# Kernel optimization log

Hardware: AMD Instinct MI355X
Metric: run time of the kernel (lower is better)

Reference implementation:

```python
import jax, jax.numpy as jnp
import numpy as np


def setup_inputs() -> dict:
    key = jax.random.key(0)
    k1, k2 = jax.random.split(key)
    N, H, K, E = 8192, 4096, 2, 64
    x = jax.random.normal(k1, (N, H), dtype=jnp.float32)
    row_idx = jnp.arange(N * K, dtype=jnp.int32).reshape(N, K)
    expert_idx = jax.random.randint(k2, (N, K), 0, E, dtype=jnp.int32)
    return {"x": x, "row_idx": row_idx, "expert_idx": expert_idx, "active_num": N * K}


def reference(x, row_idx, expert_idx, active_num):
    # x: [N, H]; row_idx, expert_idx: [N, K]
    N, H = x.shape
    K = expert_idx.shape[1]
    NK = N * K

    expert_flat = expert_idx.reshape(-1)  # [N*K]
    row_flat = row_idx.reshape(-1)        # [N*K]

    # Step 1: stable sort by expert id, carry row indices
    sorted_indices = jnp.argsort(expert_flat, stable=True)
    expanded_expert_idx = expert_flat[sorted_indices]
    dst_to_src = row_flat[sorted_indices]

    # Step 2: invert the permutation: src_to_dst[dst_to_src[i]] = i
    expanded_row_idx = jnp.zeros(NK, dtype=jnp.int32).at[dst_to_src].set(
        jnp.arange(NK, dtype=jnp.int32)
    )

    # Step 3: gather x rows; dst_to_src % N gives the original token row
    expanded_x = x[dst_to_src % N]  # [N*K, H]

    return expanded_x, expanded_row_idx, expanded_expert_idx
```

## Files before the change

kernel.cpp:

```cpp
#include <hip/hip_runtime.h>
#include <hip/hip_bf16.h>

#define TPB 256
#define NEXPERT 64

typedef float f32x4 __attribute__((ext_vector_type(4)));


__global__ void k_hist(const int* __restrict__ expert, int NK, int NB,
                       int* __restrict__ counts) {
    __shared__ int h[NEXPERT];
    const int b = blockIdx.x;
    for (int e = threadIdx.x; e < NEXPERT; e += blockDim.x) h[e] = 0;
    __syncthreads();
    const int i = b * TPB + threadIdx.x;
    if (i < NK) atomicAdd(&h[expert[i]], 1);
    __syncthreads();
    for (int e = threadIdx.x; e < NEXPERT; e += blockDim.x)
        counts[e * NB + b] = h[e];
}

__global__ void k_scan(int* __restrict__ counts, int M) {
    __shared__ int s[1024];
    const int t = threadIdx.x;
    const int nt = blockDim.x;
    const int ipt = (M + nt - 1) / nt;
    int v[8];
    int sum = 0;
    for (int j = 0; j < ipt; ++j) {
        const int idx = t * ipt + j;
        v[j] = (idx < M) ? counts[idx] : 0;
        sum += v[j];
    }
    s[t] = sum;
    __syncthreads();
    for (int off = 1; off < nt; off <<= 1) {
        const int x = (t >= off) ? s[t - off] : 0;
        __syncthreads();
        s[t] += x;
        __syncthreads();
    }
    int base = (t == 0) ? 0 : s[t - 1];
    for (int j = 0; j < ipt; ++j) {
        const int idx = t * ipt + j;
        const int c = v[j];
        if (idx < M) counts[idx] = base;
        base += c;
    }
}

__global__ void k_scatter(const int* __restrict__ expert,
                          const int* __restrict__ rowi,
                          int NK, int NB,
                          const int* __restrict__ base,
                          float* __restrict__ out_row,
                          float* __restrict__ out_expert,
                          int* __restrict__ dst_of_r) {
    __shared__ int h[TPB / 64][NEXPERT + 1];
    const int b = blockIdx.x;
    const int tid = threadIdx.x;
    const int w = tid >> 6;
    const int lane = tid & 63;
    const int i = b * TPB + tid;
    const bool valid = (i < NK);
    const int e = valid ? expert[i] : NEXPERT;

    for (int idx = tid; idx < (TPB / 64) * (NEXPERT + 1); idx += TPB)
        (&h[0][0])[idx] = 0;
    __syncthreads();

    unsigned long long mask = ~0ull;
#pragma unroll
    for (int bit = 0; bit < 7; ++bit) {
        const unsigned long long bv = __ballot((e >> bit) & 1);
        mask &= ((e >> bit) & 1) ? bv : ~bv;
    }
    const int rank_w = __popcll(mask & ((1ull << lane) - 1ull));
    const int cnt_w  = __popcll(mask);
    if (rank_w == 0) h[w][e] = cnt_w;
    __syncthreads();

    if (valid) {
        int rank = rank_w;
        for (int w2 = 0; w2 < w; ++w2) rank += h[w2][e];
        const int dst = base[e * NB + b] + rank;
        const int r = rowi[i];
        out_expert[dst] = (float)e;
        out_row[r] = (float)dst;
        dst_of_r[r] = dst;
    }
}

template <int K>
__global__ void k_gatherT(const float* __restrict__ x,
                          const int* __restrict__ dst_of_r,
                          float* __restrict__ out_x, int H, int N) {
    const int t = blockIdx.x;
    const f32x4* __restrict__ src = (const f32x4*)(x + (size_t)t * (size_t)H);
    size_t ob[K];
#pragma unroll
    for (int kk = 0; kk < K; ++kk)
        ob[kk] = (size_t)dst_of_r[t + kk * N] * (size_t)H;
    const int n4 = H >> 2;
    for (int j = threadIdx.x; j < n4; j += blockDim.x) {
        const f32x4 v = src[j];
#pragma unroll
        for (int kk = 0; kk < K; ++kk)
            __builtin_nontemporal_store(v, (f32x4*)(out_x + ob[kk]) + j);
    }
}

__global__ void k_gather_gen(const float* __restrict__ x,
                             const int* __restrict__ dst_of_r,
                             float* __restrict__ out_x, int H, int N, int K) {
    const int t = blockIdx.x;
    const f32x4* __restrict__ src = (const f32x4*)(x + (size_t)t * (size_t)H);
    const int n4 = H >> 2;
    for (int kk = 0; kk < K; ++kk) {
        const size_t ob = (size_t)dst_of_r[t + kk * N] * (size_t)H;
        for (int j = threadIdx.x; j < n4; j += blockDim.x)
            __builtin_nontemporal_store(src[j], (f32x4*)(out_x + ob) + j);
    }
}

extern "C" void kernel_launch(void* const* d_in, const int* in_sizes, int n_in,
                              void* d_out, int out_size, void* d_ws, size_t ws_size,
                              hipStream_t stream) {
    const float* x    = (const float*)d_in[0];
    const int*   rowi = (const int*)d_in[1];
    const int*   expi = (const int*)d_in[2];

    const int NK = in_sizes[1];
    const int H  = (out_size - 2 * NK) / NK;
    const int N  = in_sizes[0] / H;
    const int K  = NK / N;
    const int NB = (NK + TPB - 1) / TPB;

    float* out_x      = (float*)d_out;
    float* out_row    = out_x + (size_t)NK * (size_t)H;
    float* out_expert = out_row + NK;

    int* counts   = (int*)d_ws;
    int* dst_of_r = counts + NEXPERT * NB;

    k_hist   <<<NB, TPB, 0, stream>>>(expi, NK, NB, counts);
    k_scan   <<<1, 1024, 0, stream>>>(counts, NEXPERT * NB);
    k_scatter<<<NB, TPB, 0, stream>>>(expi, rowi, NK, NB, counts,
                                      out_row, out_expert, dst_of_r);

    switch (K) {
        case 1: k_gatherT<1><<<N, TPB, 0, stream>>>(x, dst_of_r, out_x, H, N); break;
        case 2: k_gatherT<2><<<N, TPB, 0, stream>>>(x, dst_of_r, out_x, H, N); break;
        case 3: k_gatherT<3><<<N, TPB, 0, stream>>>(x, dst_of_r, out_x, H, N); break;
        case 4: k_gatherT<4><<<N, TPB, 0, stream>>>(x, dst_of_r, out_x, H, N); break;
        default: k_gather_gen<<<N, TPB, 0, stream>>>(x, dst_of_r, out_x, H, N, K); break;
    }
}
```

Before: 77.62 us.

## Fuse prefix scan into scatter kernel, recomputing scan redundantly per block

Removes the single-block scan kernel and has every scatter block load the full histogram (64*NB counts) into shared memory and compute the exclusive prefix scan itself. This drops one kernel launch and the serial dependency on a one-block kernel. In exchange, every block redoes the whole scan and needs about 33 KB of dynamic LDS, which lowers occupancy. The scan also assumes M is divisible by TPB.

Result: faster. 75.39 us, median of 2 (-2.9%).

```diff
diff --git a/kernel.cpp b/kernel.cpp
--- a/kernel.cpp
+++ b/kernel.cpp
@@ -20,54 +20,49 @@
         counts[e * NB + b] = h[e];
 }
 
-__global__ void k_scan(int* __restrict__ counts, int M) {
-    __shared__ int s[1024];
-    const int t = threadIdx.x;
-    const int nt = blockDim.x;
-    const int ipt = (M + nt - 1) / nt;
-    int v[8];
-    int sum = 0;
-    for (int j = 0; j < ipt; ++j) {
-        const int idx = t * ipt + j;
-        v[j] = (idx < M) ? counts[idx] : 0;
-        sum += v[j];
-    }
-    s[t] = sum;
-    __syncthreads();
-    for (int off = 1; off < nt; off <<= 1) {
-        const int x = (t >= off) ? s[t - off] : 0;
-        __syncthreads();
-        s[t] += x;
-        __syncthreads();
-    }
-    int base = (t == 0) ? 0 : s[t - 1];
-    for (int j = 0; j < ipt; ++j) {
-        const int idx = t * ipt + j;
-        const int c = v[j];
-        if (idx < M) counts[idx] = base;
-        base += c;
-    }
-}
-
-__global__ void k_scatter(const int* __restrict__ expert,
-                          const int* __restrict__ rowi,
-                          int NK, int NB,
-                          const int* __restrict__ base,
-                          float* __restrict__ out_row,
-                          float* __restrict__ out_expert,
-                          int* __restrict__ dst_of_r) {
+__global__ __launch_bounds__(TPB) void k_scatter(
+    const int* __restrict__ expert, const int* __restrict__ rowi,
+    int NK, int NB, const int* __restrict__ counts,
+    float* __restrict__ out_row, float* __restrict__ out_expert,
+    int* __restrict__ dst_of_r) {
+    extern __shared__ int lds[];
     __shared__ int h[TPB / 64][NEXPERT + 1];
+    const int M = NEXPERT * NB;
+    int* cnt = lds;
+    int* s = lds + M;
     const int b = blockIdx.x;
     const int tid = threadIdx.x;
     const int w = tid >> 6;
     const int lane = tid & 63;
+
+    for (int j = tid; j < M; j += TPB) cnt[j] = counts[j];
+    for (int idx = tid; idx < (TPB / 64) * (NEXPERT + 1); idx += TPB)
+        (&h[0][0])[idx] = 0;
+    __syncthreads();
+
+    const int ipt = M / TPB;
+    const int base_i = tid * ipt;
+    int sum = 0;
+    for (int j = 0; j < ipt; ++j) sum += cnt[base_i + j];
+    s[tid] = sum;
+    __syncthreads();
+    for (int off = 1; off < TPB; off <<= 1) {
+        const int xv = (tid >= off) ? s[tid - off] : 0;
+        __syncthreads();
+        s[tid] += xv;
+        __syncthreads();
+    }
+    int run = (tid == 0) ? 0 : s[tid - 1];
+    for (int j = 0; j < ipt; ++j) {
+        const int c = cnt[base_i + j];
+        cnt[base_i + j] = run;
+        run += c;
+    }
+    __syncthreads();
+
     const int i = b * TPB + tid;
     const bool valid = (i < NK);
     const int e = valid ? expert[i] : NEXPERT;
-
-    for (int idx = tid; idx < (TPB / 64) * (NEXPERT + 1); idx += TPB)
-        (&h[0][0])[idx] = 0;
-    __syncthreads();
 
     unsigned long long mask = ~0ull;
 #pragma unroll
@@ -83,7 +78,7 @@
     if (valid) {
         int rank = rank_w;
         for (int w2 = 0; w2 < w; ++w2) rank += h[w2][e];
-        const int dst = base[e * NB + b] + rank;
+        const int dst = cnt[e * NB + b] + rank;
         const int r = rowi[i];
         out_expert[dst] = (float)e;
         out_row[r] = (float)dst;
@@ -143,10 +138,12 @@
     int* counts   = (int*)d_ws;
     int* dst_of_r = counts + NEXPERT * NB;
 
+    const int M = NEXPERT * NB;
+    const size_t lds_bytes = (size_t)(M + TPB) * sizeof(int);
+
     k_hist   <<<NB, TPB, 0, stream>>>(expi, NK, NB, counts);
-    k_scan   <<<1, 1024, 0, stream>>>(counts, NEXPERT * NB);
-    k_scatter<<<NB, TPB, 0, stream>>>(expi, rowi, NK, NB, counts,
-                                      out_row, out_expert, dst_of_r);
+    k_scatter<<<NB, TPB, lds_bytes, stream>>>(expi, rowi, NK, NB, counts,
+                                              out_row, out_expert, dst_of_r);
 
     switch (K) {
         case 1: k_gatherT<1><<<N, TPB, 0, stream>>>(x, dst_of_r, out_x, H, N); break;
```
